# Performance work log

Hardware: AMD Instinct MI355X
Metric: run time of the kernel (lower is better)

The kernel has to match this reference:

```python
import jax, jax.numpy as jnp
import numpy as np

L, D, H, HD, M = 4096, 1024, 16, 64, 4096
EPS = 1e-5


def setup_inputs() -> dict:
    key = jax.random.key(0)
    ks = jax.random.split(key, 12)
    hidden_states = jax.random.normal(ks[0], (L, D), dtype=jnp.float32)
    cu_seqlens = jnp.arange(5, dtype=jnp.int32) * (L // 4)  # [0,1024,2048,3072,4096]
    # rope freqs as cos/sin of random angles: (L, HD//2, 2)
    angles = jax.random.uniform(ks[1], (L, HD // 2), dtype=jnp.float32) * (2.0 * np.pi)
    rope_freqs = jnp.stack([jnp.cos(angles), jnp.sin(angles)], axis=-1)
    s = 0.02
    params = {
        "ln0_g": jnp.ones((D,), jnp.float32), "ln0_b": jnp.zeros((D,), jnp.float32),
        "ln1_g": jnp.ones((D,), jnp.float32), "ln1_b": jnp.zeros((D,), jnp.float32),
        "w_qkv": jax.random.normal(ks[2], (D, 3 * D), jnp.float32) * s,
        "w_o":   jax.random.normal(ks[3], (D, D), jnp.float32) * s,
        "w_fc0": jax.random.normal(ks[4], (D, M), jnp.float32) * s,
        "b_fc0": jnp.zeros((M,), jnp.float32),
        "w_fc1": jax.random.normal(ks[5], (M, D), jnp.float32) * s,
        "b_fc1": jnp.zeros((D,), jnp.float32),
    }
    return {"hidden_states": hidden_states, "cu_seqlens": cu_seqlens, "rope_freqs": rope_freqs, **params}


def _layernorm(x, g, b):
    mu = jnp.mean(x, axis=-1, keepdims=True)
    var = jnp.var(x, axis=-1, keepdims=True)
    return (x - mu) * jax.lax.rsqrt(var + EPS) * g + b


def _apply_rope(x, fc):
    # x: (L, H, HD); fc: (L, HD//2, 2) -> broadcast over heads
    xr = x.reshape(L, H, HD // 2, 2)
    a, b = xr[..., 0], xr[..., 1]
    c, s = fc[:, None, :, 0], fc[:, None, :, 1]
    out = jnp.stack([a * c - b * s, a * s + b * c], axis=-1)
    return out.reshape(L, H, HD)


def reference(hidden_states, cu_seqlens, rope_freqs, ln0_g, ln0_b, ln1_g, ln1_b,
              w_qkv, w_o, w_fc0, b_fc0, w_fc1, b_fc1):
    residual = hidden_states
    x = _layernorm(hidden_states, ln0_g, ln0_b)
    qkv = (x @ w_qkv).reshape(L, 3, H, HD)
    q, k, v = qkv[:, 0], qkv[:, 1], qkv[:, 2]
    q = _apply_rope(q, rope_freqs)
    k = _apply_rope(k, rope_freqs)
    # block-diagonal mask from cu_seqlens
    seg = jnp.searchsorted(cu_seqlens[1:], jnp.arange(L, dtype=cu_seqlens.dtype), side="right")
    mask = seg[:, None] == seg[None, :]  # (L, L)
    scale = 1.0 / np.sqrt(HD)
    scores = jnp.einsum("lhd,mhd->hlm", q, k) * scale
    scores = jnp.where(mask[None], scores, jnp.float32(-1e30))
    probs = jax.nn.softmax(scores, axis=-1)
    attn = jnp.einsum("hlm,mhd->lhd", probs, v).reshape(L, D)
    attn = attn @ w_o
    h = residual + attn
    y = _layernorm(h, ln1_g, ln1_b)
    y = jax.nn.gelu(y @ w_fc0 + b_fc0, approximate=False) @ w_fc1 + b_fc1
    return h + y
```

## Files before the change

### kernel.cpp

```cpp
#include <hip/hip_runtime.h>
#include <cstdint>
#include <cmath>

#define L_ 4096
#define D_ 1024
#define H_ 16
#define HD_ 64
#define M_ 4096

typedef __bf16 bf16_t;
typedef __attribute__((ext_vector_type(8))) __bf16 bf16x8;
typedef __attribute__((ext_vector_type(4))) __bf16 bf16x4;
typedef __attribute__((ext_vector_type(4))) float f32x4;

#define WAIT_VM0 0x0f70
#define WAIT_LGKM0 0xc07f

__device__ __forceinline__ f32x4 mfma16(bf16x8 a, bf16x8 b, f32x4 c) {
    return __builtin_amdgcn_mfma_f32_16x16x32_bf16(a, b, c, 0, 0, 0);
}

__device__ __forceinline__ void gload_lds16(const bf16_t* g, bf16_t* l) {
    __builtin_amdgcn_global_load_lds(
        (const __attribute__((address_space(1))) unsigned int*)(g),
        (__attribute__((address_space(3))) unsigned int*)(l), 16, 0, 0);
}

__device__ __forceinline__ float fast_exp2(float x) {
    float r;
    asm volatile("v_exp_f32 %0, %1" : "=v"(r) : "v"(x));
    return r;
}
__device__ __forceinline__ float fast_rcp(float x) {
    float r;
    asm volatile("v_rcp_f32 %0, %1" : "=v"(r) : "v"(x));
    return r;
}
__device__ __forceinline__ float gelu_f(float v) {
    float t = v * (0.7978845608f + 0.0356774081f * v * v);
    return v * fast_rcp(1.f + fast_exp2(-2.885390082f * t));
}

__global__ __launch_bounds__(256) void ln_kernel(const float* __restrict__ x,
                                                 const float* __restrict__ g,
                                                 const float* __restrict__ b,
                                                 bf16_t* __restrict__ out) {
    int row = blockIdx.x, tid = threadIdx.x;
    int wave = tid >> 6, lane = tid & 63;
    const f32x4* xr = (const f32x4*)(x + (long)row * D_);
    f32x4 v = xr[tid];
    float s = v.x + v.y + v.z + v.w;
    __shared__ float red[8];
#pragma unroll
    for (int off = 32; off > 0; off >>= 1) s += __shfl_down(s, off, 64);
    if (lane == 0) red[wave] = s;
    __syncthreads();
    float mean = (red[0] + red[1] + red[2] + red[3]) * (1.f / 1024.f);
    float s2 = 0.f;
#pragma unroll
    for (int i = 0; i < 4; i++) { float d = v[i] - mean; s2 += d * d; }
#pragma unroll
    for (int off = 32; off > 0; off >>= 1) s2 += __shfl_down(s2, off, 64);
    __syncthreads();
    if (lane == 0) red[wave] = s2;
    __syncthreads();
    float var = (red[0] + red[1] + red[2] + red[3]) * (1.f / 1024.f);
    float rstd = rsqrtf(var + 1e-5f);
    f32x4 g4 = ((const f32x4*)g)[tid];
    f32x4 b4 = ((const f32x4*)b)[tid];
    bf16x4 o;
#pragma unroll
    for (int i = 0; i < 4; i++) o[i] = (bf16_t)((v[i] - mean) * rstd * g4[i] + b4[i]);
    *(bf16x4*)(out + (long)row * D_ + tid * 4) = o;
}

__global__ __launch_bounds__(256) void transpose_all(
    const float* __restrict__ w_qkv, const float* __restrict__ w_o,
    const float* __restrict__ w_fc0, const float* __restrict__ w_fc1,
    bf16_t* __restrict__ t_qkv, bf16_t* __restrict__ t_o,
    bf16_t* __restrict__ t_fc0, bf16_t* __restrict__ t_fc1) {
    __shared__ float t[32][33];
    int bidx = blockIdx.x;
    const float* W;
    bf16_t* Wt;
    int K, N, tile;
    if (bidx < 3072) { W = w_qkv; Wt = t_qkv; K = 1024; N = 3072; tile = bidx; }
    else if (bidx < 4096) { W = w_o; Wt = t_o; K = 1024; N = 1024; tile = bidx - 3072; }
    else if (bidx < 8192) { W = w_fc0; Wt = t_fc0; K = 1024; N = 4096; tile = bidx - 4096; }
    else { W = w_fc1; Wt = t_fc1; K = 4096; N = 1024; tile = bidx - 8192; }
    int nt = N >> 5;
    int n0 = (tile % nt) * 32, k0 = (tile / nt) * 32;
    int tx = threadIdx.x & 31, ty = threadIdx.x >> 5;
#pragma unroll
    for (int r = 0; r < 32; r += 8)
        t[ty + r][tx] = W[(long)(k0 + ty + r) * N + n0 + tx];
    __syncthreads();
#pragma unroll
    for (int r = 0; r < 32; r += 8)
        Wt[(long)(n0 + ty + r) * K + k0 + tx] = (bf16_t)t[tx][ty + r];
}

__global__ __launch_bounds__(256) void vt_kernel(const bf16_t* __restrict__ qkv,
                                                 bf16_t* __restrict__ Vt) {
    __shared__ bf16_t t[32][33];
    int l0 = blockIdx.x * 32, c0 = blockIdx.y * 32;
    int tx = threadIdx.x & 31, ty = threadIdx.x >> 5;
#pragma unroll
    for (int r = 0; r < 32; r += 8)
        t[ty + r][tx] = qkv[(long)(l0 + ty + r) * 3072 + 2048 + c0 + tx];
    __syncthreads();
#pragma unroll
    for (int r = 0; r < 32; r += 8)
        Vt[(long)(c0 + ty + r) * 4096 + l0 + tx] = t[tx][ty + r];
}

__global__ __launch_bounds__(256) void rope_kernel(bf16_t* __restrict__ qkv,
                                                   const float* __restrict__ freqs) {
    const float k1 = 0.125f * 1.44269504089f;
    int idx = blockIdx.x * 256 + threadIdx.x;
    int g = idx & 7;
    int h = (idx >> 3) & 15;
    int l = idx >> 7;
    const float* f = freqs + (long)l * 64 + g * 8;
    f32x4 f0 = ((const f32x4*)f)[0];
    f32x4 f1 = ((const f32x4*)f)[1];
    float c[4] = {f0.x, f0.z, f1.x, f1.z};
    float s[4] = {f0.y, f0.w, f1.y, f1.w};
    bf16_t* qp = qkv + (long)l * 3072 + h * 64 + g * 8;
    bf16x8 q = *(bf16x8*)qp;
    bf16x8 k = *(bf16x8*)(qp + 1024);
    bf16x8 qo, ko;
#pragma unroll
    for (int e = 0; e < 4; e++) {
        float a = (float)q[2 * e], b = (float)q[2 * e + 1];
        qo[2 * e] = (bf16_t)((a * c[e] - b * s[e]) * k1);
        qo[2 * e + 1] = (bf16_t)((a * s[e] + b * c[e]) * k1);
        a = (float)k[2 * e]; b = (float)k[2 * e + 1];
        ko[2 * e] = (bf16_t)(a * c[e] - b * s[e]);
        ko[2 * e + 1] = (bf16_t)(a * s[e] + b * c[e]);
    }
    *(bf16x8*)qp = qo;
    *(bf16x8*)(qp + 1024) = ko;
}

#define PH_BAR1()                                        \
    __builtin_amdgcn_s_barrier();                        \
    asm volatile("s_waitcnt lgkmcnt(0)" ::: "memory");   \
    __builtin_amdgcn_s_setprio(1);

#define PH_BAR2()                                        \
    __builtin_amdgcn_s_setprio(0);                       \
    __builtin_amdgcn_s_barrier();

#define STAGE_A(d, h, kt)                                                          \
    gload_lds16(aSt + (long)((h) * 128) * K + (kt), &SA[d][h][(wv * 16) * 64]);    \
    gload_lds16(aSt + (long)((h) * 128 + 8) * K + (kt), &SA[d][h][(wv * 16 + 8) * 64]);

#define STAGE_B(d, h, kt)                                                          \
    gload_lds16(bSt + (long)((h) * 128) * K + (kt), &SB[d][h][(wv * 16) * 64]);    \
    gload_lds16(bSt + (long)((h) * 128 + 8) * K + (kt), &SB[d][h][(wv * 16 + 8) * 64]);

#define RD_A(dst, src, rq)                                                          \
    _Pragma("unroll") for (int i_ = 0; i_ < 4; i_++) {                              \
        dst[i_][0] = *(const bf16x8*)&src[((rq) * 64 + i_ * 16 + l16) * 64 + sl0 * 8]; \
        dst[i_][1] = *(const bf16x8*)&src[((rq) * 64 + i_ * 16 + l16) * 64 + sl1 * 8]; \
    }

#define RD_B(dst, src, cq)                                                          \
    _Pragma("unroll") for (int j_ = 0; j_ < 2; j_++) {                              \
        dst[j_][0] = *(const bf16x8*)&src[(bro + (cq) * 32 + j_ * 16 + l16) * 64 + sl0 * 8]; \
        dst[j_][1] = *(const bf16x8*)&src[(bro + (cq) * 32 + j_ * 16 + l16) * 64 + sl1 * 8]; \
    }

#define MFMA_Q(rq, cq, Af, Bf)                                                      \
    _Pragma("unroll") for (int i_ = 0; i_ < 4; i_++)                                \
    _Pragma("unroll") for (int j_ = 0; j_ < 2; j_++) {                              \
        acc[(rq) * 4 + i_][(cq) * 2 + j_] =                                         \
            mfma16(Af[i_][0], Bf[j_][0], acc[(rq) * 4 + i_][(cq) * 2 + j_]);        \
        acc[(rq) * 4 + i_][(cq) * 2 + j_] =                                         \
            mfma16(Af[i_][1], Bf[j_][1], acc[(rq) * 4 + i_][(cq) * 2 + j_]);        \
    }

template <int EPI>
__device__ __forceinline__ void gemm256_core(
    const bf16_t* __restrict__ A, const bf16_t* __restrict__ Bt,
    int K, int N, long bm, long bn, int kb, int ke,
    bf16_t* __restrict__ outB, const float* __restrict__ bias) {
    __shared__ __align__(16) bf16_t SA[2][2][128 * 64];
    __shared__ __align__(16) bf16_t SB[2][2][128 * 64];
    int tid = threadIdx.x;
    int wv = tid >> 6, lane = tid & 63;
    int quad = lane >> 4, l16 = lane & 15;
    int wm = wv >> 2, wn = wv & 3;
    int lr = lane >> 3;
    int sc = (lane & 7) ^ (lr & 7);
    int sl0 = quad ^ (l16 & 7);
    int sl1 = (4 + quad) ^ (l16 & 7);
    int bro = (wn & 1) * 64;

    const bf16_t* aSt = A + (bm + wv * 16 + lr) * (long)K + sc * 8;
    const bf16_t* bSt = Bt + (bn + wv * 16 + lr) * (long)K + sc * 8;
    const bf16_t* pa0 = SA[0][wm];
    const bf16_t* pa1 = SA[1][wm];
    const bf16_t* pb0 = SB[0][wn >> 1];
    const bf16_t* pb1 = SB[1][wn >> 1];

    f32x4 acc[8][4];
#pragma unroll
    for (int i = 0; i < 8; i++)
#pragma unroll
        for (int j = 0; j < 4; j++) acc[i][j] = (f32x4){0.f, 0.f, 0.f, 0.f};

    bf16x8 a0[4][2], a1[4][2], b0[2][2], b1[2][2];

    STAGE_B(0, 0, kb); STAGE_A(0, 0, kb); STAGE_B(0, 1, kb); STAGE_A(0, 1, kb);
    STAGE_B(1, 0, kb + 64); STAGE_A(1, 0, kb + 64); STAGE_B(1, 1, kb + 64);
    asm volatile("s_waitcnt vmcnt(6)" ::: "memory");
    __builtin_amdgcn_s_barrier();
    RD_B(b0, pb0, 0);

    for (int k0 = kb; k0 < ke; k0 += 128) {
        int kt2 = (k0 + 128 < ke) ? k0 + 128 : kb;
        int kt3 = kt2 + 64;
        RD_A(a0, pa0, 0); RD_B(b1, pb0, 1);
        STAGE_A(1, 1, k0 + 64);
        PH_BAR1(); MFMA_Q(0, 0, a0, b0); PH_BAR2();
        RD_A(a1, pa0, 1);
        STAGE_B(0, 0, kt2);
        PH_BAR1(); MFMA_Q(0, 1, a0, b1); PH_BAR2();
        STAGE_A(0, 0, kt2);
        asm volatile("s_waitcnt vmcnt(4)" ::: "memory");
        PH_BAR1(); MFMA_Q(1, 0, a1, b0); PH_BAR2();
        RD_B(b0, pb1, 0);
        STAGE_B(0, 1, kt2);
        PH_BAR1(); MFMA_Q(1, 1, a1, b1); PH_BAR2();
        RD_A(a0, pa1, 0); RD_B(b1, pb1, 1);
        STAGE_A(0, 1, kt2);
        PH_BAR1(); MFMA_Q(0, 0, a0, b0); PH_BAR2();
        RD_A(a1, pa1, 1);
        STAGE_B(1, 0, kt3);
        PH_BAR1(); MFMA_Q(0, 1, a0, b1); PH_BAR2();
        STAGE_A(1, 0, kt3);
        asm volatile("s_waitcnt vmcnt(4)" ::: "memory");
        PH_BAR1(); MFMA_Q(1, 0, a1, b0); PH_BAR2();
        RD_B(b0, pb0, 0);
        STAGE_B(1, 1, kt3);
        PH_BAR1(); MFMA_Q(1, 1, a1, b1); PH_BAR2();
    }
    asm volatile("s_waitcnt vmcnt(0)" ::: "memory");

#pragma unroll
    for (int ri = 0; ri < 8; ri++)
#pragma unroll
        for (int cj = 0; cj < 4; cj++)
#pragma unroll
            for (int r = 0; r < 4; r++) {
                long row = bm + wm * 128 + (ri >> 2) * 64 + (ri & 3) * 16 + quad * 4 + r;
                long col = bn + wn * 64 + (cj >> 1) * 32 + (cj & 1) * 16 + l16;
                long idx = row * (long)N + col;
                float v = acc[ri][cj][r];
                if (EPI == 0) {
                    outB[idx] = (bf16_t)v;
                } else {
                    v += bias[col];
                    outB[idx] = (bf16_t)gelu_f(v);
                }
            }
}

__global__ __launch_bounds__(512) void gemm256_qkv(const bf16_t* __restrict__ A,
                                                   const bf16_t* __restrict__ Bt,
                                                   bf16_t* __restrict__ outB) {
    int g = blockIdx.x & 7, w = blockIdx.x >> 3;
    int gm = g >> 2, gn = g & 3;
    long bm = (long)(gm * 8 + w / 3) * 256;
    long bn = (long)(gn * 3 + w % 3) * 256;
    gemm256_core<0>(A, Bt, 1024, 3072, bm, bn, 0, 1024, outB, nullptr);
}

__global__ __launch_bounds__(512) void gemm256_fc0(const bf16_t* __restrict__ A,
                                                   const bf16_t* __restrict__ Bt,
                                                   bf16_t* __restrict__ outB,
                                                   const float* __restrict__ bias) {
    int g = blockIdx.x & 7, w = blockIdx.x >> 3;
    int gm = g >> 2, gn = g & 3;
    long bm = (long)(gm * 8 + (w >> 2)) * 256;
    long bn = (long)(gn * 4 + (w & 3)) * 256;
    gemm256_core<2>(A, Bt, 1024, 4096, bm, bn, 0, 1024, outB, bias);
}

__global__ __launch_bounds__(512) void gemm256_fc1(const bf16_t* __restrict__ A,
                                                   const bf16_t* __restrict__ Bt,
                                                   bf16_t* __restrict__ P) {
    int g = blockIdx.x & 7, w = blockIdx.x >> 3;
    int z = g >> 1, gm = g & 1;
    long bm = (long)(gm * 8 + (w >> 2)) * 256;
    long bn = (long)(w & 3) * 256;
    gemm256_core<0>(A, Bt, 4096, 1024, bm, bn, z * 1024, z * 1024 + 1024,
                    P + (long)z * L_ * D_, nullptr);
}

__global__ __launch_bounds__(256) void reduce_fc1(const bf16_t* __restrict__ P,
                                                  const float* __restrict__ bias,
                                                  float* __restrict__ out) {
    long i = (long)blockIdx.x * 256 + threadIdx.x;
    f32x4 b = ((const f32x4*)bias)[i & 255];
    f32x4 v = ((f32x4*)out)[i];
#pragma unroll
    for (int z = 0; z < 4; z++) {
        bf16x4 p = ((const bf16x4*)(P + (long)z * L_ * D_))[i];
#pragma unroll
        for (int e = 0; e < 4; e++) v[e] += (float)p[e];
    }
    v.x += b.x; v.y += b.y; v.z += b.z; v.w += b.w;
    ((f32x4*)out)[i] = v;
}

__global__ __launch_bounds__(256) void gemm_bt64_res(const bf16_t* __restrict__ A,
                                                     const bf16_t* __restrict__ Bt,
                                                     int M, int N, int K,
                                                     float* __restrict__ outF,
                                                     const float* __restrict__ res) {
    __shared__ __align__(16) bf16_t As[128 * 64];
    __shared__ __align__(16) bf16_t Bs[64 * 64];
    int tid = threadIdx.x;
    int wave = tid >> 6, lane = tid & 63;
    int quad = lane >> 4, l16 = lane & 15;

    int g = blockIdx.x & 7, w = blockIdx.x >> 3;
    int bn_i = w & 15, bm_i = g * 4 + (w >> 4);
    long bm = (long)bm_i * 128, bn = (long)bn_i * 64;

    f32x4 acc[2][4];
#pragma unroll
    for (int i = 0; i < 2; i++)
#pragma unroll
        for (int j = 0; j < 4; j++) acc[i][j] = (f32x4){0.f, 0.f, 0.f, 0.f};

    int lr = lane >> 3;
    int sc = (lane & 7) ^ (lr & 7);
    const bf16_t* a_base = A + (bm + wave * 32 + lr) * (long)K + sc * 8;
    const bf16_t* b_base = Bt + (bn + wave * 16 + lr) * (long)K + sc * 8;

    for (int k0 = 0; k0 < K; k0 += 64) {
        __syncthreads();
#pragma unroll
        for (int i = 0; i < 4; i++)
            gload_lds16(a_base + k0 + (long)(8 * i) * K, &As[(wave * 32 + 8 * i) * 64]);
#pragma unroll
        for (int i = 0; i < 2; i++)
            gload_lds16(b_base + k0 + (long)(8 * i) * K, &Bs[(wave * 16 + 8 * i) * 64]);
        __builtin_amdgcn_s_waitcnt(WAIT_VM0);
        __syncthreads();

#pragma unroll
        for (int h = 0; h < 2; h++) {
            int sl = (h * 4 + quad) ^ (l16 & 7);
            bf16x8 af[2], bfr[4];
#pragma unroll
            for (int i = 0; i < 2; i++)
                af[i] = *(const bf16x8*)&As[(wave * 32 + i * 16 + l16) * 64 + sl * 8];
#pragma unroll
            for (int j = 0; j < 4; j++)
                bfr[j] = *(const bf16x8*)&Bs[(j * 16 + l16) * 64 + sl * 8];
#pragma unroll
            for (int i = 0; i < 2; i++)
#pragma unroll
                for (int j = 0; j < 4; j++)
                    acc[i][j] = mfma16(af[i], bfr[j], acc[i][j]);
        }
    }

#pragma unroll
    for (int i = 0; i < 2; i++)
#pragma unroll
        for (int j = 0; j < 4; j++)
#pragma unroll
            for (int r = 0; r < 4; r++) {
                long row = bm + wave * 32 + i * 16 + quad * 4 + r;
                long col = bn + j * 16 + l16;
                long idx = row * (long)N + col;
                outF[idx] = acc[i][j][r] + res[idx];
            }
}

__global__ __launch_bounds__(256) void attn_kernel(const bf16_t* __restrict__ qkv,
                                                   const bf16_t* __restrict__ Vt,
                                                   const int* __restrict__ cu,
                                                   bf16_t* __restrict__ out) {
    __shared__ __align__(16) bf16_t QPs[4 * 16 * 72];
    __shared__ __align__(16) bf16_t Ks[2][64 * 64];
    __shared__ __align__(16) bf16_t Vs[2][64 * 64];

    int tid = threadIdx.x, wave = tid >> 6, lane = tid & 63;
    int quad = lane >> 4, l16 = lane & 15;

    int g = blockIdx.x & 7, w = blockIdx.x >> 3;
    int head = (w & 1) * 8 + g;
    int qt = (w >> 1) & 15;
    int seg = w >> 5;
    int s0 = cu[seg], s1 = cu[seg + 1];
    int r0 = s0 + qt * 64;
    const long hoff = (long)head * 64;

    bf16_t* Qs = QPs;
    bf16_t* Psw = &QPs[wave * 16 * 72];

    int lr = lane >> 3;
    int sc = (lane & 7) ^ (lr & 7);
    int sl0 = (0 * 4 + quad) ^ (l16 & 7);
    int sl1 = (1 * 4 + quad) ^ (l16 & 7);

#pragma unroll
    for (int i = 0; i < 2; i++) {
        int row = wave * 16 + i * 8 + lr;
        gload_lds16(qkv + (long)(r0 + row) * 3072 + hoff + sc * 8,
                    &Qs[(wave * 16 + i * 8) * 64]);
    }
    __builtin_amdgcn_s_waitcnt(WAIT_VM0);
    __syncthreads();
    bf16x8 aq0 = *(const bf16x8*)&Qs[(wave * 16 + l16) * 64 + sl0 * 8];
    bf16x8 aq1 = *(const bf16x8*)&Qs[(wave * 16 + l16) * 64 + sl1 * 8];

    bf16x8 ones;
#pragma unroll
    for (int e = 0; e < 8; e++) ones[e] = (bf16_t)1.0f;

    f32x4 o[4];
#pragma unroll
    for (int j = 0; j < 4; j++) o[j] = (f32x4){0.f, 0.f, 0.f, 0.f};
    f32x4 lacc = (f32x4){0.f, 0.f, 0.f, 0.f};

    for (int kt = s0; kt < s1; kt += 128) {
        __syncthreads();
#pragma unroll
        for (int i = 0; i < 2; i++) {
            int row = wave * 16 + i * 8 + lr;
            long kr0 = (long)(kt + row) * 3072 + 1024 + hoff + sc * 8;
            gload_lds16(qkv + kr0, &Ks[0][(wave * 16 + i * 8) * 64]);
            gload_lds16(qkv + kr0 + (long)64 * 3072, &Ks[1][(wave * 16 + i * 8) * 64]);
            long vr0 = (hoff + row) * (long)4096 + kt + sc * 8;
            gload_lds16(Vt + vr0, &Vs[0][(wave * 16 + i * 8) * 64]);
            gload_lds16(Vt + vr0 + 64, &Vs[1][(wave * 16 + i * 8) * 64]);
        }
        __builtin_amdgcn_s_waitcnt(WAIT_VM0);
        __syncthreads();

#pragma unroll
        for (int half = 0; half < 2; half++) {
            f32x4 sacc[4];
#pragma unroll
            for (int j = 0; j < 4; j++) sacc[j] = (f32x4){0.f, 0.f, 0.f, 0.f};
#pragma unroll
            for (int j = 0; j < 4; j++) {
                bf16x8 b0 = *(const bf16x8*)&Ks[half][(j * 16 + l16) * 64 + sl0 * 8];
                bf16x8 b1 = *(const bf16x8*)&Ks[half][(j * 16 + l16) * 64 + sl1 * 8];
                sacc[j] = mfma16(aq0, b0, sacc[j]);
                sacc[j] = mfma16(aq1, b1, sacc[j]);
            }

#pragma unroll
            for (int j = 0; j < 4; j++)
#pragma unroll
                for (int r = 0; r < 4; r++)
                    Psw[(quad * 4 + r) * 72 + j * 16 + l16] = (bf16_t)fast_exp2(sacc[j][r]);

            __builtin_amdgcn_s_waitcnt(WAIT_LGKM0);

            bf16x8 ap0 = *(const bf16x8*)&Psw[l16 * 72 + 0 * 32 + quad * 8];
            bf16x8 ap1 = *(const bf16x8*)&Psw[l16 * 72 + 1 * 32 + quad * 8];
#pragma unroll
            for (int j2 = 0; j2 < 4; j2++) {
                bf16x8 b0 = *(const bf16x8*)&Vs[half][(j2 * 16 + l16) * 64 + sl0 * 8];
                bf16x8 b1 = *(const bf16x8*)&Vs[half][(j2 * 16 + l16) * 64 + sl1 * 8];
                o[j2] = mfma16(ap0, b0, o[j2]);
                o[j2] = mfma16(ap1, b1, o[j2]);
            }
            lacc = mfma16(ap0, ones, lacc);
            lacc = mfma16(ap1, ones, lacc);
        }
    }

#pragma unroll
    for (int r = 0; r < 4; r++) {
        float inv = fast_rcp(lacc[r]);
        int row = r0 + wave * 16 + quad * 4 + r;
#pragma unroll
        for (int j2 = 0; j2 < 4; j2++)
            out[(long)row * 1024 + head * 64 + j2 * 16 + l16] = (bf16_t)(o[j2][r] * inv);
    }
}

extern "C" void kernel_launch(void* const* d_in, const int* in_sizes, int n_in,
                              void* d_out, int out_size, void* d_ws, size_t ws_size,
                              hipStream_t stream) {
    const float* hidden = (const float*)d_in[0];
    const int* cu = (const int*)d_in[1];
    const float* freqs = (const float*)d_in[2];
    const float* ln0_g = (const float*)d_in[3];
    const float* ln0_b = (const float*)d_in[4];
    const float* ln1_g = (const float*)d_in[5];
    const float* ln1_b = (const float*)d_in[6];
    const float* w_qkv = (const float*)d_in[7];
    const float* w_o = (const float*)d_in[8];
    const float* w_fc0 = (const float*)d_in[9];
    const float* b_fc0 = (const float*)d_in[10];
    const float* w_fc1 = (const float*)d_in[11];
    const float* b_fc1 = (const float*)d_in[12];
    float* out = (float*)d_out;

    char* ws = (char*)d_ws;
    bf16_t* qkv = (bf16_t*)(ws);
    bf16_t* attn = (bf16_t*)(ws + ((size_t)24 << 20));
    bf16_t* act = (bf16_t*)(ws);
    bf16_t* x_bf = (bf16_t*)(ws + ((size_t)32 << 20));
    bf16_t* Vt = x_bf;
    bf16_t* y_bf = x_bf;
    bf16_t* fc1p = (bf16_t*)(ws + ((size_t)40 << 20));
    bf16_t* wqkvT = (bf16_t*)(ws + ((size_t)72 << 20));
    bf16_t* woT = (bf16_t*)(ws + ((size_t)78 << 20));
    bf16_t* wfc0T = (bf16_t*)(ws + ((size_t)80 << 20));
    bf16_t* wfc1T = (bf16_t*)(ws + ((size_t)88 << 20));
    float* h = out;

    transpose_all<<<12288, 256, 0, stream>>>(w_qkv, w_o, w_fc0, w_fc1,
                                             wqkvT, woT, wfc0T, wfc1T);

    ln_kernel<<<L_, 256, 0, stream>>>(hidden, ln0_g, ln0_b, x_bf);

    gemm256_qkv<<<192, 512, 0, stream>>>(x_bf, wqkvT, qkv);

    rope_kernel<<<(L_ * H_ * 8) / 256, 256, 0, stream>>>(qkv, freqs);
    vt_kernel<<<dim3(4096 / 32, 1024 / 32), 256, 0, stream>>>(qkv, Vt);

    attn_kernel<<<1024, 256, 0, stream>>>(qkv, Vt, cu, attn);

    gemm_bt64_res<<<512, 256, 0, stream>>>(
        attn, woT, L_, 1024, 1024, h, hidden);

    ln_kernel<<<L_, 256, 0, stream>>>(h, ln1_g, ln1_b, y_bf);

    gemm256_fc0<<<256, 512, 0, stream>>>(y_bf, wfc0T, act, b_fc0);

    gemm256_fc1<<<256, 512, 0, stream>>>(act, wfc1T, fc1p);
    reduce_fc1<<<(L_ * D_ / 4) / 256, 256, 0, stream>>>(fc1p, b_fc1, out);
}
```

Before: 328.2 us.

## Restructure 256x256 GEMM mainloop to 32-wide K tiles with smaller LDS

Rewrites the shared bf16 GEMM core so each stage loads a 256x32 K-slice of A and B, where it previously used two 128x64 halves. This cuts LDS use from 128KB to 64KB. Each wave now reads four B fragments and issues one MFMA per fragment pair per K-step, using a new XOR swizzle and matching epilogue column mapping. The aim is lower LDS pressure, possibly higher occupancy, and a simpler double-buffered schedule. In exchange it takes twice as many loop iterations and barriers per K and uses full vmcnt(0) waits, which may expose global load latency.

```diff
diff --git a/kernel.cpp b/kernel.cpp
--- a/kernel.cpp
+++ b/kernel.cpp
@@ -152,58 +152,44 @@
     __builtin_amdgcn_s_setprio(0);                       \
     __builtin_amdgcn_s_barrier();
 
-#define STAGE_A(d, h, kt)                                                          \
-    gload_lds16(aSt + (long)((h) * 128) * K + (kt), &SA[d][h][(wv * 16) * 64]);    \
-    gload_lds16(aSt + (long)((h) * 128 + 8) * K + (kt), &SA[d][h][(wv * 16 + 8) * 64]);
-
-#define STAGE_B(d, h, kt)                                                          \
-    gload_lds16(bSt + (long)((h) * 128) * K + (kt), &SB[d][h][(wv * 16) * 64]);    \
-    gload_lds16(bSt + (long)((h) * 128 + 8) * K + (kt), &SB[d][h][(wv * 16 + 8) * 64]);
-
-#define RD_A(dst, src, rq)                                                          \
-    _Pragma("unroll") for (int i_ = 0; i_ < 4; i_++) {                              \
-        dst[i_][0] = *(const bf16x8*)&src[((rq) * 64 + i_ * 16 + l16) * 64 + sl0 * 8]; \
-        dst[i_][1] = *(const bf16x8*)&src[((rq) * 64 + i_ * 16 + l16) * 64 + sl1 * 8]; \
-    }
-
-#define RD_B(dst, src, cq)                                                          \
-    _Pragma("unroll") for (int j_ = 0; j_ < 2; j_++) {                              \
-        dst[j_][0] = *(const bf16x8*)&src[(bro + (cq) * 32 + j_ * 16 + l16) * 64 + sl0 * 8]; \
-        dst[j_][1] = *(const bf16x8*)&src[(bro + (cq) * 32 + j_ * 16 + l16) * 64 + sl1 * 8]; \
-    }
-
-#define MFMA_Q(rq, cq, Af, Bf)                                                      \
-    _Pragma("unroll") for (int i_ = 0; i_ < 4; i_++)                                \
-    _Pragma("unroll") for (int j_ = 0; j_ < 2; j_++) {                              \
-        acc[(rq) * 4 + i_][(cq) * 2 + j_] =                                         \
-            mfma16(Af[i_][0], Bf[j_][0], acc[(rq) * 4 + i_][(cq) * 2 + j_]);        \
-        acc[(rq) * 4 + i_][(cq) * 2 + j_] =                                         \
-            mfma16(Af[i_][1], Bf[j_][1], acc[(rq) * 4 + i_][(cq) * 2 + j_]);        \
-    }
+#define STG_A32(d, kt)                                               \
+    gload_lds16(aSt + (kt), &SA[d][(wv * 32) * 32]);                 \
+    gload_lds16(aSt + (long)16 * K + (kt), &SA[d][(wv * 32 + 16) * 32]);
+
+#define STG_B32(d, kt)                                               \
+    gload_lds16(bSt + (kt), &SB[d][(wv * 32) * 32]);                 \
+    gload_lds16(bSt + (long)16 * K + (kt), &SB[d][(wv * 32 + 16) * 32]);
+
+#define RD_A4(dst, d, fo)                                                       \
+    _Pragma("unroll") for (int f_ = 0; f_ < 4; f_++)                            \
+        dst[f_] = *(const bf16x8*)&SA[d][(wm * 128 + ((fo) + f_) * 16 + l16) * 32 + rsl * 8];
+
+#define RD_B4(dst, d)                                                           \
+    _Pragma("unroll") for (int j_ = 0; j_ < 4; j_++)                            \
+        dst[j_] = *(const bf16x8*)&SB[d][(wn * 64 + j_ * 16 + l16) * 32 + rsl * 8];
+
+#define MFMA_H(base, aF, bF)                                                    \
+    _Pragma("unroll") for (int i_ = 0; i_ < 4; i_++)                            \
+    _Pragma("unroll") for (int j_ = 0; j_ < 4; j_++)                            \
+        acc[(base) + i_][j_] = mfma16(aF[i_], bF[j_], acc[(base) + i_][j_]);
 
 template <int EPI>
 __device__ __forceinline__ void gemm256_core(
     const bf16_t* __restrict__ A, const bf16_t* __restrict__ Bt,
     int K, int N, long bm, long bn, int kb, int ke,
     bf16_t* __restrict__ outB, const float* __restrict__ bias) {
-    __shared__ __align__(16) bf16_t SA[2][2][128 * 64];
-    __shared__ __align__(16) bf16_t SB[2][2][128 * 64];
+    __shared__ __align__(16) bf16_t SA[2][256 * 32];
+    __shared__ __align__(16) bf16_t SB[2][256 * 32];
     int tid = threadIdx.x;
     int wv = tid >> 6, lane = tid & 63;
     int quad = lane >> 4, l16 = lane & 15;
     int wm = wv >> 2, wn = wv & 3;
-    int lr = lane >> 3;
-    int sc = (lane & 7) ^ (lr & 7);
-    int sl0 = quad ^ (l16 & 7);
-    int sl1 = (4 + quad) ^ (l16 & 7);
-    int bro = (wn & 1) * 64;
-
-    const bf16_t* aSt = A + (bm + wv * 16 + lr) * (long)K + sc * 8;
-    const bf16_t* bSt = Bt + (bn + wv * 16 + lr) * (long)K + sc * 8;
-    const bf16_t* pa0 = SA[0][wm];
-    const bf16_t* pa1 = SA[1][wm];
-    const bf16_t* pb0 = SB[0][wn >> 1];
-    const bf16_t* pb1 = SB[1][wn >> 1];
+    int rsl = quad ^ (l16 & 3);
+
+    int sr = lane >> 2;
+    int ssl = (lane & 3) ^ (sr & 3);
+    const bf16_t* aSt = A + (bm + wv * 32 + sr) * (long)K + ssl * 8;
+    const bf16_t* bSt = Bt + (bn + wv * 32 + sr) * (long)K + ssl * 8;
 
     f32x4 acc[8][4];
 #pragma unroll
@@ -211,41 +197,29 @@
 #pragma unroll
         for (int j = 0; j < 4; j++) acc[i][j] = (f32x4){0.f, 0.f, 0.f, 0.f};
 
-    bf16x8 a0[4][2], a1[4][2], b0[2][2], b1[2][2];
-
-    STAGE_B(0, 0, kb); STAGE_A(0, 0, kb); STAGE_B(0, 1, kb); STAGE_A(0, 1, kb);
-    STAGE_B(1, 0, kb + 64); STAGE_A(1, 0, kb + 64); STAGE_B(1, 1, kb + 64);
-    asm volatile("s_waitcnt vmcnt(6)" ::: "memory");
+    bf16x8 aL[4], aH[4], b0[4], b1[4];
+
+    STG_A32(0, kb); STG_B32(0, kb);
+    STG_A32(1, kb + 32); STG_B32(1, kb + 32);
+    asm volatile("s_waitcnt vmcnt(4)" ::: "memory");
     __builtin_amdgcn_s_barrier();
-    RD_B(b0, pb0, 0);
-
-    for (int k0 = kb; k0 < ke; k0 += 128) {
-        int kt2 = (k0 + 128 < ke) ? k0 + 128 : kb;
-        int kt3 = kt2 + 64;
-        RD_A(a0, pa0, 0); RD_B(b1, pb0, 1);
-        STAGE_A(1, 1, k0 + 64);
-        PH_BAR1(); MFMA_Q(0, 0, a0, b0); PH_BAR2();
-        RD_A(a1, pa0, 1);
-        STAGE_B(0, 0, kt2);
-        PH_BAR1(); MFMA_Q(0, 1, a0, b1); PH_BAR2();
-        STAGE_A(0, 0, kt2);
-        asm volatile("s_waitcnt vmcnt(4)" ::: "memory");
-        PH_BAR1(); MFMA_Q(1, 0, a1, b0); PH_BAR2();
-        RD_B(b0, pb1, 0);
-        STAGE_B(0, 1, kt2);
-        PH_BAR1(); MFMA_Q(1, 1, a1, b1); PH_BAR2();
-        RD_A(a0, pa1, 0); RD_B(b1, pb1, 1);
-        STAGE_A(0, 1, kt2);
-        PH_BAR1(); MFMA_Q(0, 0, a0, b0); PH_BAR2();
-        RD_A(a1, pa1, 1);
-        STAGE_B(1, 0, kt3);
-        PH_BAR1(); MFMA_Q(0, 1, a0, b1); PH_BAR2();
-        STAGE_A(1, 0, kt3);
-        asm volatile("s_waitcnt vmcnt(4)" ::: "memory");
-        PH_BAR1(); MFMA_Q(1, 0, a1, b0); PH_BAR2();
-        RD_B(b0, pb0, 0);
-        STAGE_B(1, 1, kt3);
-        PH_BAR1(); MFMA_Q(1, 1, a1, b1); PH_BAR2();
+    RD_A4(aL, 0, 0); RD_B4(b0, 0);
+
+    for (int k0 = kb; k0 < ke; k0 += 64) {
+        int kt2 = (k0 + 64 < ke) ? k0 + 64 : kb;
+        int kt3 = (k0 + 64 < ke) ? k0 + 96 : kb + 32;
+        RD_A4(aH, 0, 4);
+        asm volatile("s_waitcnt vmcnt(0)" ::: "memory");
+        PH_BAR1(); MFMA_H(0, aL, b0); PH_BAR2();
+        RD_B4(b1, 1); RD_A4(aL, 1, 0);
+        STG_A32(0, kt2); STG_B32(0, kt2);
+        PH_BAR1(); MFMA_H(4, aH, b0); PH_BAR2();
+        RD_A4(aH, 1, 4);
+        asm volatile("s_waitcnt vmcnt(0)" ::: "memory");
+        PH_BAR1(); MFMA_H(0, aL, b1); PH_BAR2();
+        RD_B4(b0, 0); RD_A4(aL, 0, 0);
+        STG_A32(1, kt3); STG_B32(1, kt3);
+        PH_BAR1(); MFMA_H(4, aH, b1); PH_BAR2();
     }
     asm volatile("s_waitcnt vmcnt(0)" ::: "memory");
 
@@ -256,7 +230,7 @@
 #pragma unroll
             for (int r = 0; r < 4; r++) {
                 long row = bm + wm * 128 + (ri >> 2) * 64 + (ri & 3) * 16 + quad * 4 + r;
-                long col = bn + wn * 64 + (cj >> 1) * 32 + (cj & 1) * 16 + l16;
+                long col = bn + wn * 64 + cj * 16 + l16;
                 long idx = row * (long)N + col;
                 float v = acc[ri][cj][r];
                 if (EPI == 0) {
```

Result: slower. 350.7 us (+6.9%).

## Restructure GEMM ping-pong schedule to one barrier per phase with prefetched fragments

Applied to the files above, without the earlier changes.

Reorders the main GEMM loop so each phase issues one barrier, then its global-to-LDS stage, then the MFMA block. The LDS fragment reads for the next phase now follow the MFMAs, and a lgkmcnt wait sits at the end of each phase. This halves the barrier count per phase and lets LDS reads overlap the other waves' compute. It changes where the LDS hazard protection falls, which risks a race if the stage writes and the reads are not fully separated.

```diff
diff --git a/kernel.cpp b/kernel.cpp
--- a/kernel.cpp
+++ b/kernel.cpp
@@ -143,15 +143,6 @@
     *(bf16x8*)(qp + 1024) = ko;
 }
 
-#define PH_BAR1()                                        \
-    __builtin_amdgcn_s_barrier();                        \
-    asm volatile("s_waitcnt lgkmcnt(0)" ::: "memory");   \
-    __builtin_amdgcn_s_setprio(1);
-
-#define PH_BAR2()                                        \
-    __builtin_amdgcn_s_setprio(0);                       \
-    __builtin_amdgcn_s_barrier();
-
 #define STAGE_A(d, h, kt)                                                          \
     gload_lds16(aSt + (long)((h) * 128) * K + (kt), &SA[d][h][(wv * 16) * 64]);    \
     gload_lds16(aSt + (long)((h) * 128 + 8) * K + (kt), &SA[d][h][(wv * 16 + 8) * 64]);
@@ -180,6 +171,12 @@
         acc[(rq) * 4 + i_][(cq) * 2 + j_] =                                         \
             mfma16(Af[i_][1], Bf[j_][1], acc[(rq) * 4 + i_][(cq) * 2 + j_]);        \
     }
+
+#define LGKM0() asm volatile("s_waitcnt lgkmcnt(0)" ::: "memory")
+#define VMC(n) asm volatile("s_waitcnt vmcnt(" #n ")" ::: "memory")
+#define BAR() __builtin_amdgcn_s_barrier()
+#define PRIO1() __builtin_amdgcn_s_setprio(1)
+#define PRIO0() __builtin_amdgcn_s_setprio(0)
 
 template <int EPI>
 __device__ __forceinline__ void gemm256_core(
@@ -215,39 +212,40 @@
 
     STAGE_B(0, 0, kb); STAGE_A(0, 0, kb); STAGE_B(0, 1, kb); STAGE_A(0, 1, kb);
     STAGE_B(1, 0, kb + 64); STAGE_A(1, 0, kb + 64); STAGE_B(1, 1, kb + 64);
-    asm volatile("s_waitcnt vmcnt(6)" ::: "memory");
-    __builtin_amdgcn_s_barrier();
-    RD_B(b0, pb0, 0);
+    VMC(6);
+    BAR();
+    RD_A(a0, pa0, 0); RD_B(b0, pb0, 0);
+    LGKM0();
 
     for (int k0 = kb; k0 < ke; k0 += 128) {
         int kt2 = (k0 + 128 < ke) ? k0 + 128 : kb;
         int kt3 = kt2 + 64;
-        RD_A(a0, pa0, 0); RD_B(b1, pb0, 1);
-        STAGE_A(1, 1, k0 + 64);
-        PH_BAR1(); MFMA_Q(0, 0, a0, b0); PH_BAR2();
-        RD_A(a1, pa0, 1);
-        STAGE_B(0, 0, kt2);
-        PH_BAR1(); MFMA_Q(0, 1, a0, b1); PH_BAR2();
-        STAGE_A(0, 0, kt2);
-        asm volatile("s_waitcnt vmcnt(4)" ::: "memory");
-        PH_BAR1(); MFMA_Q(1, 0, a1, b0); PH_BAR2();
-        RD_B(b0, pb1, 0);
-        STAGE_B(0, 1, kt2);
-        PH_BAR1(); MFMA_Q(1, 1, a1, b1); PH_BAR2();
-        RD_A(a0, pa1, 0); RD_B(b1, pb1, 1);
-        STAGE_A(0, 1, kt2);
-        PH_BAR1(); MFMA_Q(0, 0, a0, b0); PH_BAR2();
-        RD_A(a1, pa1, 1);
-        STAGE_B(1, 0, kt3);
-        PH_BAR1(); MFMA_Q(0, 1, a0, b1); PH_BAR2();
-        STAGE_A(1, 0, kt3);
-        asm volatile("s_waitcnt vmcnt(4)" ::: "memory");
-        PH_BAR1(); MFMA_Q(1, 0, a1, b0); PH_BAR2();
-        RD_B(b0, pb0, 0);
-        STAGE_B(1, 1, kt3);
-        PH_BAR1(); MFMA_Q(1, 1, a1, b1); PH_BAR2();
-    }
-    asm volatile("s_waitcnt vmcnt(0)" ::: "memory");
+        BAR(); STAGE_A(1, 1, k0 + 64);
+        PRIO1(); MFMA_Q(0, 0, a0, b0); PRIO0();
+        RD_B(b1, pb0, 1); LGKM0();
+        BAR(); STAGE_B(0, 0, kt2);
+        PRIO1(); MFMA_Q(0, 1, a0, b1); PRIO0();
+        RD_A(a1, pa0, 1); LGKM0();
+        BAR(); STAGE_A(0, 0, kt2);
+        PRIO1(); MFMA_Q(1, 0, a1, b0); PRIO0();
+        VMC(4);
+        BAR(); STAGE_B(0, 1, kt2);
+        PRIO1(); MFMA_Q(1, 1, a1, b1); PRIO0();
+        RD_A(a0, pa1, 0); RD_B(b0, pb1, 0); LGKM0();
+        BAR(); STAGE_A(0, 1, kt2);
+        PRIO1(); MFMA_Q(0, 0, a0, b0); PRIO0();
+        RD_B(b1, pb1, 1); LGKM0();
+        BAR(); STAGE_B(1, 0, kt3);
+        PRIO1(); MFMA_Q(0, 1, a0, b1); PRIO0();
+        RD_A(a1, pa1, 1); LGKM0();
+        BAR(); STAGE_A(1, 0, kt3);
+        PRIO1(); MFMA_Q(1, 0, a1, b0); PRIO0();
+        VMC(4);
+        BAR(); STAGE_B(1, 1, kt3);
+        PRIO1(); MFMA_Q(1, 1, a1, b1); PRIO0();
+        RD_A(a0, pa0, 0); RD_B(b0, pb0, 0); LGKM0();
+    }
+    VMC(0);
 
 #pragma unroll
     for (int ri = 0; ri < 8; ri++)
```

New measurement: 314.2 us. -4.3%, faster.
